# Optimization experiments

Measured on AMD Instinct MI355X. Metric: run time of the kernel, lower is better.

Reference implementation:

```python
import jax, jax.numpy as jnp
import numpy as np

B, T, C = 4, 2048, 1024


def setup_inputs() -> dict:
    key = jax.random.key(0)
    ks = jax.random.split(key, 5)
    s = 1.0 / np.sqrt(C)
    return {
        "X": jax.random.normal(ks[0], (B, T, C), dtype=jnp.float32),
        "Wq": jax.random.normal(ks[1], (C, C), dtype=jnp.float32) * s,
        "Wk": jax.random.normal(ks[2], (C, C), dtype=jnp.float32) * s,
        "Wv": jax.random.normal(ks[3], (C, C), dtype=jnp.float32) * s,
        "Wo": jax.random.normal(ks[4], (C, C), dtype=jnp.float32) * s,
    }


def reference(X, Wq, Wk, Wv, Wo):
    Bx, Tx, Cx = X.shape
    Q = X @ Wq  # [B,T,C]
    K = X @ Wk
    V = X @ Wv
    scores = jnp.einsum('btc,bsc->bts', Q, K) / jnp.sqrt(jnp.asarray(Cx, X.dtype))
    # causal mask: position t attends to s <= t
    causal = jnp.tril(jnp.ones((Tx, Tx), dtype=bool))
    scores = jnp.where(causal, scores, jnp.asarray(-jnp.inf, scores.dtype))
    weights = jax.nn.softmax(scores, axis=-1)
    out = jnp.einsum('bts,bsc->btc', weights, V)
    return out @ Wo
```

## Files before the change

kernel.cpp:

```cpp
#include <hip/hip_runtime.h>
#include <hip/hip_bf16.h>
#include <cmath>


typedef __attribute__((ext_vector_type(8))) __bf16 bf16x8;
typedef __attribute__((ext_vector_type(8))) short short8;
typedef __attribute__((ext_vector_type(4))) float f32x4;

__device__ __forceinline__ unsigned short f2bf(float f) {
  union { float f; unsigned u; } v; v.f = f;
  unsigned u = v.u;
  u += ((u >> 16) & 1u) + 0x7fffu;
  return (unsigned short)(u >> 16);
}
__device__ __forceinline__ float bf2f(unsigned short h) {
  union { unsigned u; float f; } v; v.u = ((unsigned)h) << 16;
  return v.f;
}

#define GLDS(gp, sp)                                                           \
  __builtin_amdgcn_global_load_lds(                                            \
      (const __attribute__((address_space(1))) void*)(gp),                     \
      (__attribute__((address_space(3))) void*)(sp), 16, 0, 0)

__global__ void cast_kernel(const float* __restrict__ src,
                            unsigned short* __restrict__ dst, int n) {
  int i = (blockIdx.x * blockDim.x + threadIdx.x) * 4;
  if (i >= n) return;
  float4 f = *(const float4*)(src + i);
  ushort4 o = make_ushort4(f2bf(f.x), f2bf(f.y), f2bf(f.z), f2bf(f.w));
  *(ushort4*)(dst + i) = o;
}

__global__ void transpose4(const float* __restrict__ w0,
                           const float* __restrict__ w1,
                           const float* __restrict__ w2,
                           const float* __restrict__ w3,
                           unsigned short* __restrict__ wcat,
                           unsigned short* __restrict__ wot,
                           int n) {
  const float* src = blockIdx.z == 0 ? w0 : blockIdx.z == 1 ? w1
                     : blockIdx.z == 2 ? w2 : w3;
  unsigned short* dst = blockIdx.z < 3 ? wcat + (size_t)blockIdx.z * n * n : wot;
  __shared__ float tile[32][33];
  int bx = blockIdx.x * 32, by = blockIdx.y * 32;
  int tx = threadIdx.x, ty = threadIdx.y;
#pragma unroll
  for (int i = 0; i < 32; i += 8)
    tile[ty + i][tx] = src[(size_t)(by + ty + i) * n + bx + tx];
  __syncthreads();
#pragma unroll
  for (int i = 0; i < 32; i += 8)
    dst[(size_t)(bx + ty + i) * n + by + tx] = f2bf(tile[tx][ty + i]);
}

template <typename OutT>
__global__ __launch_bounds__(256, 2)
void gemm_bt(const unsigned short* __restrict__ A, int lda, long long sA,
             const unsigned short* __restrict__ B, int ldb, long long sB,
             OutT* __restrict__ Cp, int ldc, long long sC,
             int K, float alpha, int tri, int kcap, int gx, int qkv) {
  A  += (long long)blockIdx.z * sA;
  B  += (long long)blockIdx.z * sB;
  Cp += (long long)blockIdx.z * sC;

  int by, bx;
  if (tri) {
    const int idx = blockIdx.x;
    by = (int)((sqrtf(8.f * idx + 1.f) - 1.f) * 0.5f);
    while (by * (by + 1) / 2 > idx) --by;
    while ((by + 1) * (by + 2) / 2 <= idx) ++by;
    bx = idx - by * (by + 1) / 2;
  } else if (gx > 0) {
    const int id = blockIdx.x;
    const int gs = gx * 8;
    const int g = id / gs, r = id - g * gs;
    bx = r >> 3;
    by = g * 8 + (r & 7);
  } else {
    by = blockIdx.y;
    bx = blockIdx.x;
  }
  const int m0 = by * 128;
  const int n0 = bx * 128;
  const int Keff = kcap ? min(K, m0 + 128) : K;

  const int tid  = threadIdx.x;
  const int lane = tid & 63;
  const int w    = tid >> 6;
  const int wm   = (w >> 1) * 64;
  const int wn   = (w & 1) * 64;
  const int quad = lane >> 4;
  const int l16  = lane & 15;

  __shared__ unsigned short As[128 * 64];
  __shared__ unsigned short Bs[128 * 64];

  f32x4 acc[4][4];
#pragma unroll
  for (int i = 0; i < 4; ++i)
#pragma unroll
    for (int j = 0; j < 4; ++j)
      acc[i][j] = (f32x4){0.f, 0.f, 0.f, 0.f};

  const int srow = tid >> 3;
  const int scol = ((tid & 7) ^ (srow & 7)) * 8;
  const unsigned short* gA = A + (long long)(m0 + srow) * lda + scol;
  const unsigned short* gB = B + (long long)(n0 + srow) * ldb + scol;
  const int rsw = l16 & 7;

  for (int kt = 0; kt < Keff; kt += 64) {
    __syncthreads();
#pragma unroll
    for (int r = 0; r < 4; ++r) {
      GLDS(gA + (long long)(r * 32) * lda + kt, As + r * 2048 + tid * 8);
      GLDS(gB + (long long)(r * 32) * ldb + kt, Bs + r * 2048 + tid * 8);
    }
    __syncthreads();
#pragma unroll
    for (int ks = 0; ks < 2; ++ks) {
      bf16x8 af[4], bfr[4];
#pragma unroll
      for (int i = 0; i < 4; ++i)
        af[i] = *(const bf16x8*)(As + (wm + i * 16 + l16) * 64 +
                                 ((ks * 4 + quad) ^ rsw) * 8);
#pragma unroll
      for (int j = 0; j < 4; ++j)
        bfr[j] = *(const bf16x8*)(Bs + (wn + j * 16 + l16) * 64 +
                                  ((ks * 4 + quad) ^ rsw) * 8);
#pragma unroll
      for (int i = 0; i < 4; ++i)
#pragma unroll
        for (int j = 0; j < 4; ++j)
          acc[i][j] = __builtin_amdgcn_mfma_f32_16x16x32_bf16(af[i], bfr[j],
                                                              acc[i][j], 0, 0, 0);
    }
  }

#pragma unroll
  for (int i = 0; i < 4; ++i) {
#pragma unroll
    for (int j = 0; j < 4; ++j) {
      const int row = m0 + wm + i * 16 + quad * 4;
      const int col = n0 + wn + j * 16 + l16;
      if constexpr (sizeof(OutT) == 2) {
        if (qkv) {
          if (col >= 2048) {
            const int b = row >> 11, t = row & 2047, cv = col - 2048;
            ushort4 o = make_ushort4(f2bf(acc[i][j][0]), f2bf(acc[i][j][1]),
                                     f2bf(acc[i][j][2]), f2bf(acc[i][j][3]));
            *(ushort4*)((unsigned short*)Cp + 16777216LL +
                        ((long long)(b * 1024 + cv)) * 2048 + t) = o;
          } else {
            unsigned short* dst =
                (unsigned short*)Cp + (col >= 1024 ? 8388608LL - 1024 : 0);
#pragma unroll
            for (int r = 0; r < 4; ++r)
              dst[(long long)(row + r) * 1024 + col] = f2bf(acc[i][j][r]);
          }
          continue;
        }
#pragma unroll
        for (int r = 0; r < 4; ++r)
          Cp[(long long)(row + r) * ldc + col] = (OutT)f2bf(acc[i][j][r] * alpha);
      } else {
#pragma unroll
        for (int r = 0; r < 4; ++r)
          Cp[(long long)(row + r) * ldc + col] = acc[i][j][r] * alpha;
      }
    }
  }
}

__global__ __launch_bounds__(256)
void softmax_causal(unsigned short* __restrict__ S, int T) {
  const long long row = blockIdx.x;
  const int t = (int)(row & (long long)(T - 1));
  const int limit = ((t >> 7) + 1) << 7;
  unsigned short* p = S + row * T;
  const int tid  = threadIdx.x;
  const int base = tid * 8;
  const bool active = base < limit;

  short8 raw = {};
  if (active) raw = *(const short8*)(p + base);
  float x[8];
  float mx = -1e30f;
#pragma unroll
  for (int j = 0; j < 8; ++j) {
    bool valid = active && (base + j) <= t;
    x[j] = valid ? bf2f((unsigned short)raw[j]) : -1e30f;
    mx = fmaxf(mx, x[j]);
  }
#pragma unroll
  for (int off = 32; off > 0; off >>= 1) mx = fmaxf(mx, __shfl_xor(mx, off));
  __shared__ float red[8];
  const int wv = tid >> 6;
  if ((tid & 63) == 0) red[wv] = mx;
  __syncthreads();
  mx = fmaxf(fmaxf(red[0], red[1]), fmaxf(red[2], red[3]));

  float sum = 0.f;
#pragma unroll
  for (int j = 0; j < 8; ++j) {
    bool valid = active && (base + j) <= t;
    x[j] = valid ? __expf(x[j] - mx) : 0.f;
    sum += x[j];
  }
#pragma unroll
  for (int off = 32; off > 0; off >>= 1) sum += __shfl_xor(sum, off);
  if ((tid & 63) == 0) red[4 + wv] = sum;
  __syncthreads();
  sum = red[4] + red[5] + red[6] + red[7];
  const float inv = 1.f / sum;

  if (active) {
    unsigned short out[8];
#pragma unroll
    for (int j = 0; j < 8; ++j) out[j] = f2bf(x[j] * inv);
    *(short8*)(p + base) = *(const short8*)out;
  }
}

extern "C" void kernel_launch(void* const* d_in, const int* in_sizes, int n_in,
                              void* d_out, int out_size, void* d_ws,
                              size_t ws_size, hipStream_t stream) {
  (void)in_sizes; (void)n_in; (void)out_size; (void)ws_size;
  const int Bb = 4, T = 2048, C = 1024;
  const int M = Bb * T;

  const float* X  = (const float*)d_in[0];
  const float* Wq = (const float*)d_in[1];
  const float* Wk = (const float*)d_in[2];
  const float* Wv = (const float*)d_in[3];
  const float* Wo = (const float*)d_in[4];
  float* Out = (float*)d_out;

  char* w = (char*)d_ws;
  unsigned short* Xb   = (unsigned short*)w; w += (size_t)M * C * 2;
  unsigned short* Wcat = (unsigned short*)w; w += (size_t)3 * C * C * 2;
  unsigned short* Wot  = (unsigned short*)w; w += (size_t)C * C * 2;
  unsigned short* Q    = (unsigned short*)w; w += (size_t)M * C * 2;
  unsigned short* Kb   = (unsigned short*)w; w += (size_t)M * C * 2;
  unsigned short* Vt   = (unsigned short*)w; w += (size_t)M * C * 2;
  unsigned short* O    = Xb;
  unsigned short* S    = (unsigned short*)d_out;

  cast_kernel<<<(M * C) / 4 / 256, 256, 0, stream>>>(X, Xb, M * C);
  transpose4<<<dim3(C / 32, C / 32, 4), dim3(32, 8), 0, stream>>>(
      Wq, Wk, Wv, Wo, Wcat, Wot, C);

  dim3 blk(256);
  gemm_bt<unsigned short><<<dim3((3 * C / 128) * (M / 128), 1, 1), blk, 0, stream>>>(
      Xb, C, 0, Wcat, C, 0, Q, C, 0, C, 1.f, 0, 0, 3 * C / 128, 1);
  const int ntri = (T / 128) * (T / 128 + 1) / 2;
  gemm_bt<unsigned short><<<dim3(ntri, 1, Bb), blk, 0, stream>>>(
      Q, C, (long long)T * C, Kb, C, (long long)T * C,
      S, T, (long long)T * T, C, 0.03125f, 1, 0, 0, 0);
  softmax_causal<<<M, 256, 0, stream>>>(S, T);
  gemm_bt<unsigned short><<<dim3((C / 128) * (T / 128), 1, Bb), blk, 0, stream>>>(
      S, T, (long long)T * T, Vt, T, (long long)C * T,
      O, C, (long long)T * C, T, 1.f, 0, 1, C / 128, 0);
  gemm_bt<float><<<dim3((C / 128) * (M / 128), 1, 1), blk, 0, stream>>>(
      O, C, 0, Wot, C, 0, Out, C, 0, C, 1.f, 0, 0, C / 128, 0);
}
```

Baseline: 274.9 us.

## Merge prep kernels, add 8-wave GEMM variant, reverse causal PV block order

Folds the cast and weight-transpose kernels into one prep launch to save a launch. Templates the GEMM on wave count and runs the QK^T, PV and output projections with 512-thread blocks, each wave owning a 32x64 sub-tile. This lowers per-wave accumulator registers and raises waves per block for better latency hiding, at the cost of more LDS read traffic per MFMA. The causal-capped PV GEMM now schedules the longest row tiles first to reduce tail imbalance.

```diff
diff --git a/kernel.cpp b/kernel.cpp
--- a/kernel.cpp
+++ b/kernel.cpp
@@ -23,39 +23,40 @@
       (const __attribute__((address_space(1))) void*)(gp),                     \
       (__attribute__((address_space(3))) void*)(sp), 16, 0, 0)
 
-__global__ void cast_kernel(const float* __restrict__ src,
-                            unsigned short* __restrict__ dst, int n) {
-  int i = (blockIdx.x * blockDim.x + threadIdx.x) * 4;
-  if (i >= n) return;
-  float4 f = *(const float4*)(src + i);
-  ushort4 o = make_ushort4(f2bf(f.x), f2bf(f.y), f2bf(f.z), f2bf(f.w));
-  *(ushort4*)(dst + i) = o;
-}
-
-__global__ void transpose4(const float* __restrict__ w0,
-                           const float* __restrict__ w1,
-                           const float* __restrict__ w2,
-                           const float* __restrict__ w3,
-                           unsigned short* __restrict__ wcat,
-                           unsigned short* __restrict__ wot,
-                           int n) {
-  const float* src = blockIdx.z == 0 ? w0 : blockIdx.z == 1 ? w1
-                     : blockIdx.z == 2 ? w2 : w3;
-  unsigned short* dst = blockIdx.z < 3 ? wcat + (size_t)blockIdx.z * n * n : wot;
-  __shared__ float tile[32][33];
-  int bx = blockIdx.x * 32, by = blockIdx.y * 32;
-  int tx = threadIdx.x, ty = threadIdx.y;
-#pragma unroll
-  for (int i = 0; i < 32; i += 8)
-    tile[ty + i][tx] = src[(size_t)(by + ty + i) * n + bx + tx];
-  __syncthreads();
-#pragma unroll
-  for (int i = 0; i < 32; i += 8)
-    dst[(size_t)(bx + ty + i) * n + by + tx] = f2bf(tile[tx][ty + i]);
-}
-
-template <typename OutT>
-__global__ __launch_bounds__(256, 2)
+__global__ void prep(const float* __restrict__ X,
+                     const float* __restrict__ w0, const float* __restrict__ w1,
+                     const float* __restrict__ w2, const float* __restrict__ w3,
+                     unsigned short* __restrict__ Xb,
+                     unsigned short* __restrict__ wcat,
+                     unsigned short* __restrict__ wot,
+                     int n) {
+  if (blockIdx.z < 4) {
+    const float* src = blockIdx.z == 0 ? w0 : blockIdx.z == 1 ? w1
+                       : blockIdx.z == 2 ? w2 : w3;
+    unsigned short* dst =
+        blockIdx.z < 3 ? wcat + (size_t)blockIdx.z * n * n : wot;
+    __shared__ float tile[32][33];
+    int bx = blockIdx.x * 32, by = blockIdx.y * 32;
+    int tx = threadIdx.x, ty = threadIdx.y;
+#pragma unroll
+    for (int i = 0; i < 32; i += 8)
+      tile[ty + i][tx] = src[(size_t)(by + ty + i) * n + bx + tx];
+    __syncthreads();
+#pragma unroll
+    for (int i = 0; i < 32; i += 8)
+      dst[(size_t)(bx + ty + i) * n + by + tx] = f2bf(tile[tx][ty + i]);
+  } else {
+    const int bid = (blockIdx.z - 4) * 1024 + blockIdx.y * 32 + blockIdx.x;
+    const int t = threadIdx.y * 32 + threadIdx.x;
+    const int i = (bid * 256 + t) * 4;
+    float4 f = *(const float4*)(X + i);
+    ushort4 o = make_ushort4(f2bf(f.x), f2bf(f.y), f2bf(f.z), f2bf(f.w));
+    *(ushort4*)(Xb + i) = o;
+  }
+}
+
+template <typename OutT, int NW>
+__global__ __launch_bounds__(NW * 64, NW / 2)
 void gemm_bt(const unsigned short* __restrict__ A, int lda, long long sA,
              const unsigned short* __restrict__ B, int ldb, long long sB,
              OutT* __restrict__ Cp, int ldc, long long sC,
@@ -77,6 +78,7 @@
     const int g = id / gs, r = id - g * gs;
     bx = r >> 3;
     by = g * 8 + (r & 7);
+    if (kcap) by = (gridDim.x / gx) - 1 - by;
   } else {
     by = blockIdx.y;
     bx = blockIdx.x;
@@ -88,17 +90,19 @@
   const int tid  = threadIdx.x;
   const int lane = tid & 63;
   const int w    = tid >> 6;
-  const int wm   = (w >> 1) * 64;
+  const int wm   = (NW == 4) ? (w >> 1) * 64 : (w >> 1) * 32;
   const int wn   = (w & 1) * 64;
   const int quad = lane >> 4;
   const int l16  = lane & 15;
-
-  __shared__ unsigned short As[128 * 64];
-  __shared__ unsigned short Bs[128 * 64];
-
-  f32x4 acc[4][4];
-#pragma unroll
-  for (int i = 0; i < 4; ++i)
+  constexpr int AI = (NW == 4) ? 4 : 2;
+  constexpr int NR = 128 / (NW * 8);
+
+  __shared__ unsigned short As[8192];
+  __shared__ unsigned short Bs[8192];
+
+  f32x4 acc[AI][4];
+#pragma unroll
+  for (int i = 0; i < AI; ++i)
 #pragma unroll
     for (int j = 0; j < 4; ++j)
       acc[i][j] = (f32x4){0.f, 0.f, 0.f, 0.f};
@@ -112,16 +116,16 @@
   for (int kt = 0; kt < Keff; kt += 64) {
     __syncthreads();
 #pragma unroll
-    for (int r = 0; r < 4; ++r) {
-      GLDS(gA + (long long)(r * 32) * lda + kt, As + r * 2048 + tid * 8);
-      GLDS(gB + (long long)(r * 32) * ldb + kt, Bs + r * 2048 + tid * 8);
+    for (int r = 0; r < NR; ++r) {
+      GLDS(gA + (long long)(r * NW * 8) * lda + kt, As + r * NW * 512 + tid * 8);
+      GLDS(gB + (long long)(r * NW * 8) * ldb + kt, Bs + r * NW * 512 + tid * 8);
     }
     __syncthreads();
 #pragma unroll
     for (int ks = 0; ks < 2; ++ks) {
-      bf16x8 af[4], bfr[4];
-#pragma unroll
-      for (int i = 0; i < 4; ++i)
+      bf16x8 af[AI], bfr[4];
+#pragma unroll
+      for (int i = 0; i < AI; ++i)
         af[i] = *(const bf16x8*)(As + (wm + i * 16 + l16) * 64 +
                                  ((ks * 4 + quad) ^ rsw) * 8);
 #pragma unroll
@@ -129,7 +133,7 @@
         bfr[j] = *(const bf16x8*)(Bs + (wn + j * 16 + l16) * 64 +
                                   ((ks * 4 + quad) ^ rsw) * 8);
 #pragma unroll
-      for (int i = 0; i < 4; ++i)
+      for (int i = 0; i < AI; ++i)
 #pragma unroll
         for (int j = 0; j < 4; ++j)
           acc[i][j] = __builtin_amdgcn_mfma_f32_16x16x32_bf16(af[i], bfr[j],
@@ -138,7 +142,7 @@
   }
 
 #pragma unroll
-  for (int i = 0; i < 4; ++i) {
+  for (int i = 0; i < AI; ++i) {
 #pragma unroll
     for (int j = 0; j < 4; ++j) {
       const int row = m0 + wm + i * 16 + quad * 4;
@@ -246,21 +250,21 @@
   unsigned short* O    = Xb;
   unsigned short* S    = (unsigned short*)d_out;
 
-  cast_kernel<<<(M * C) / 4 / 256, 256, 0, stream>>>(X, Xb, M * C);
-  transpose4<<<dim3(C / 32, C / 32, 4), dim3(32, 8), 0, stream>>>(
-      Wq, Wk, Wv, Wo, Wcat, Wot, C);
-
-  dim3 blk(256);
-  gemm_bt<unsigned short><<<dim3((3 * C / 128) * (M / 128), 1, 1), blk, 0, stream>>>(
+  prep<<<dim3(32, 32, 12), dim3(32, 8), 0, stream>>>(X, Wq, Wk, Wv, Wo, Xb,
+                                                     Wcat, Wot, C);
+
+  gemm_bt<unsigned short, 4><<<dim3((3 * C / 128) * (M / 128), 1, 1), dim3(256),
+                               0, stream>>>(
       Xb, C, 0, Wcat, C, 0, Q, C, 0, C, 1.f, 0, 0, 3 * C / 128, 1);
   const int ntri = (T / 128) * (T / 128 + 1) / 2;
-  gemm_bt<unsigned short><<<dim3(ntri, 1, Bb), blk, 0, stream>>>(
+  gemm_bt<unsigned short, 8><<<dim3(ntri, 1, Bb), dim3(512), 0, stream>>>(
       Q, C, (long long)T * C, Kb, C, (long long)T * C,
       S, T, (long long)T * T, C, 0.03125f, 1, 0, 0, 0);
   softmax_causal<<<M, 256, 0, stream>>>(S, T);
-  gemm_bt<unsigned short><<<dim3((C / 128) * (T / 128), 1, Bb), blk, 0, stream>>>(
+  gemm_bt<unsigned short, 8><<<dim3((C / 128) * (T / 128), 1, Bb), dim3(512), 0,
+                               stream>>>(
       S, T, (long long)T * T, Vt, T, (long long)C * T,
       O, C, (long long)T * C, T, 1.f, 0, 1, C / 128, 0);
-  gemm_bt<float><<<dim3((C / 128) * (M / 128), 1, 1), blk, 0, stream>>>(
+  gemm_bt<float, 8><<<dim3((C / 128) * (M / 128), 1, 1), dim3(512), 0, stream>>>(
       O, C, 0, Wot, C, 0, Out, C, 0, C, 1.f, 0, 0, C / 128, 0);
 }
```

Result: no change. 270.3 us (-1.7%).
